# Optimization experiments

Measured on AMD Instinct MI355X. Metric: run time of the kernel, lower is better.

The kernel has to match this reference:

```python
import jax, jax.numpy as jnp
import numpy as np

N_NODES = 100000
N_EDGES = 800000
IN_DIM = 128
HIDDEN_DIM = 256
OUT_DIM = 40


def setup_inputs() -> dict:
    key = jax.random.key(0)
    k_x, k_e, k_w1, k_w2 = jax.random.split(key, 4)
    x = jax.random.normal(k_x, (N_NODES, IN_DIM), dtype=jnp.float32)
    edge_index = jax.random.randint(k_e, (2, N_EDGES), 0, N_NODES, dtype=jnp.int32)
    # Glorot-style init like PyG GCNConv
    s1 = 1.0 / np.sqrt(IN_DIM)
    s2 = 1.0 / np.sqrt(HIDDEN_DIM)
    W1 = jax.random.uniform(k_w1, (IN_DIM, HIDDEN_DIM), dtype=jnp.float32, minval=-s1, maxval=s1)
    b1 = jnp.zeros((HIDDEN_DIM,), dtype=jnp.float32)
    W2 = jax.random.uniform(k_w2, (HIDDEN_DIM, OUT_DIM), dtype=jnp.float32, minval=-s2, maxval=s2)
    b2 = jnp.zeros((OUT_DIM,), dtype=jnp.float32)
    return {"x": x, "edge_index": edge_index, "W1": W1, "b1": b1, "W2": W2, "b2": b2}


def _gcn_conv(x, W, b, src, dst, n_nodes):
    # PyG GCNConv: linear transform, add self-loops, symmetric normalization,
    # scatter-add aggregation, then bias.
    h = x @ W  # [N, F_out]
    loops = jnp.arange(n_nodes, dtype=src.dtype)
    s = jnp.concatenate([src, loops])  # [E+N]
    d = jnp.concatenate([dst, loops])
    deg = jax.ops.segment_sum(jnp.ones_like(d, dtype=h.dtype), d, num_segments=n_nodes)
    dinv = jax.lax.rsqrt(jnp.maximum(deg, 1.0))  # deg >= 1 with self-loops
    norm = dinv[s] * dinv[d]  # [E+N]
    msgs = h[s] * norm[:, None]  # [E+N, F_out] -- dominant memory traffic
    out = jax.ops.segment_sum(msgs, d, num_segments=n_nodes)
    return out + b


def reference(x, edge_index, W1, b1, W2, b2):
    src, dst = edge_index[0], edge_index[1]
    n = x.shape[0]
    h = _gcn_conv(x, W1, b1, src, dst, n)
    h = jax.nn.relu(h)
    # dropout is identity in eval mode
    h = _gcn_conv(h, W2, b2, src, dst, n)
    return jax.nn.log_softmax(h, axis=1)
```

## Files before the change

### kernel.cpp

```cpp
#include <hip/hip_runtime.h>
#include <math.h>

#define N_NODES 100000
#define N_EDGES 800000
#define IN_DIM 128
#define HIDDEN_DIM 256
#define OUT_DIM 40
#define CAP 32
#define SHARD_DIV 12500
#define NPAIRS (N_NODES * 64)
#define T1 (HIDDEN_DIM * IN_DIM)
#define T2 (64 * HIDDEN_DIM)

typedef __attribute__((ext_vector_type(8))) __bf16 bf16x8;
typedef __attribute__((ext_vector_type(4))) float f32x4;

#define FIXSC 131072.0f
#define FIXSC_INV 7.62939453125e-6f

__device__ __forceinline__ unsigned short f2bf(float f) {
    unsigned u = __float_as_uint(f);
    unsigned r = (u + 0x7FFFu + ((u >> 16) & 1u)) >> 16;
    return (unsigned short)r;
}
__device__ __forceinline__ float bflo(unsigned v) { return __uint_as_float(v << 16); }
__device__ __forceinline__ float bfhi(unsigned v) { return __uint_as_float(v & 0xFFFF0000u); }

__device__ __forceinline__ bf16x8 ld_frag16(const unsigned short* p) {
    union { uint4 u; bf16x8 b; } t;
    t.u = *(const uint4*)p;
    return t.b;
}

__global__ __launch_bounds__(256) void fill_kernel(const int* __restrict__ src,
                                                   const int* __restrict__ dst,
                                                   int* __restrict__ cnt,
                                                   int* __restrict__ esrc, int e) {
    int shard = blockIdx.x & 7;
    int i = (blockIdx.x >> 3) * 256 + threadIdx.x;
    if (i < e) {
        int d = dst[i];
        if (d / SHARD_DIV == shard) {
            int p = atomicAdd(&cnt[d], 1);
            if (p < CAP) esrc[d * CAP + p] = src[i];
        }
    }
}

__global__ __launch_bounds__(256) void cast_kernel(const float* __restrict__ x,
                                                   const int* __restrict__ cnt,
                                                   unsigned* __restrict__ xs,
                                                   const float* __restrict__ W1,
                                                   unsigned short* __restrict__ W1t,
                                                   const float* __restrict__ W2,
                                                   unsigned short* __restrict__ W2t) {
    int i = blockIdx.x * 256 + threadIdx.x;
    if (i < NPAIRS) {
        float dn = rsqrtf((float)cnt[i >> 6] + 1.0f) * FIXSC;
        float2 v = ((const float2*)x)[i];
        xs[i] = (unsigned)f2bf(v.x * dn) | ((unsigned)f2bf(v.y * dn) << 16);
    }
    if (i < T1) {
        int n = i >> 7, k = i & 127;
        W1t[i] = f2bf(W1[(size_t)k * HIDDEN_DIM + n]);
    } else if (i < T1 + T2) {
        int j = i - T1;
        int n = j >> 8, k = j & 255;
        float v = (n < OUT_DIM) ? W2[(size_t)k * OUT_DIM + n] : 0.0f;
        W2t[j] = f2bf(v);
    }
}

__global__ __launch_bounds__(256) void aggx_kernel(const unsigned* __restrict__ xs,
                                                   const int* __restrict__ cnt,
                                                   const int* __restrict__ esrc,
                                                   unsigned* __restrict__ aggxb, int n) {
    int wid = (blockIdx.x * 256 + threadIdx.x) >> 6;
    int lane = threadIdx.x & 63;
    if (wid >= n) return;
    int c = cnt[wid];
    int m = c < CAP ? c : CAP;
    unsigned v = xs[(size_t)wid * 64 + lane];
    int ia = (int)bflo(v), ib = (int)bfhi(v);
    int base = wid * CAP;
    int j = 0;
    for (; j + 7 < m; j += 8) {
        int s0 = esrc[base + j],     s1 = esrc[base + j + 1];
        int s2 = esrc[base + j + 2], s3 = esrc[base + j + 3];
        int s4 = esrc[base + j + 4], s5 = esrc[base + j + 5];
        int s6 = esrc[base + j + 6], s7 = esrc[base + j + 7];
        unsigned u0 = xs[(size_t)s0 * 64 + lane];
        unsigned u1 = xs[(size_t)s1 * 64 + lane];
        unsigned u2 = xs[(size_t)s2 * 64 + lane];
        unsigned u3 = xs[(size_t)s3 * 64 + lane];
        unsigned u4 = xs[(size_t)s4 * 64 + lane];
        unsigned u5 = xs[(size_t)s5 * 64 + lane];
        unsigned u6 = xs[(size_t)s6 * 64 + lane];
        unsigned u7 = xs[(size_t)s7 * 64 + lane];
        ia += ((int)bflo(u0) + (int)bflo(u1)) + ((int)bflo(u2) + (int)bflo(u3))
            + ((int)bflo(u4) + (int)bflo(u5)) + ((int)bflo(u6) + (int)bflo(u7));
        ib += ((int)bfhi(u0) + (int)bfhi(u1)) + ((int)bfhi(u2) + (int)bfhi(u3))
            + ((int)bfhi(u4) + (int)bfhi(u5)) + ((int)bfhi(u6) + (int)bfhi(u7));
    }
    for (; j + 3 < m; j += 4) {
        int s0 = esrc[base + j],     s1 = esrc[base + j + 1];
        int s2 = esrc[base + j + 2], s3 = esrc[base + j + 3];
        unsigned u0 = xs[(size_t)s0 * 64 + lane];
        unsigned u1 = xs[(size_t)s1 * 64 + lane];
        unsigned u2 = xs[(size_t)s2 * 64 + lane];
        unsigned u3 = xs[(size_t)s3 * 64 + lane];
        ia += ((int)bflo(u0) + (int)bflo(u1)) + ((int)bflo(u2) + (int)bflo(u3));
        ib += ((int)bfhi(u0) + (int)bfhi(u1)) + ((int)bfhi(u2) + (int)bfhi(u3));
    }
    for (; j < m; j++) {
        unsigned u = xs[(size_t)esrc[base + j] * 64 + lane];
        ia += (int)bflo(u); ib += (int)bfhi(u);
    }
    float k = rsqrtf((float)c + 1.0f) * FIXSC_INV;
    float ax = (float)ia * k, ay = (float)ib * k;
    aggxb[(size_t)wid * 64 + lane] = (unsigned)f2bf(ax) | ((unsigned)f2bf(ay) << 16);
}

#define BSTR 40
#define HSTR 136
__global__ __launch_bounds__(256) void gemm12_kernel(const unsigned short* __restrict__ A,
                                                     const unsigned short* __restrict__ W1t,
                                                     const unsigned short* __restrict__ W2t,
                                                     const float* __restrict__ b1,
                                                     const int* __restrict__ cnt,
                                                     unsigned short* __restrict__ h2s,
                                                     int M) {
    __shared__ __align__(16) unsigned short Bs[256 * BSTR];
    __shared__ __align__(16) unsigned short Hs[4 * 32 * HSTR];
    int tid = threadIdx.x;
    int wv = tid >> 6, lane = tid & 63;
    int quad = lane >> 4, l16 = lane & 15;
    int m0 = blockIdx.x * 128;

    float bv[16];
#pragma unroll
    for (int ct = 0; ct < 16; ct++) bv[ct] = b1[ct * 16 + l16];

    f32x4 zero4 = {0.f, 0.f, 0.f, 0.f};
    f32x4 acc[2][16];
#pragma unroll
    for (int rt = 0; rt < 2; rt++)
#pragma unroll
        for (int ct = 0; ct < 16; ct++) acc[rt][ct] = zero4;

    for (int k0 = 0; k0 < 128; k0 += 32) {
#pragma unroll
        for (int rep = 0; rep < 4; rep++) {
            int lin = rep * 256 + tid;
            int row = lin >> 2, ch = lin & 3;
            *(uint4*)&Bs[row * BSTR + ch * 8] =
                *(const uint4*)&W1t[(size_t)row * 128 + k0 + ch * 8];
        }
        __syncthreads();
        bf16x8 af[2];
#pragma unroll
        for (int rt = 0; rt < 2; rt++) {
            int gm = m0 + wv * 32 + rt * 16 + l16;
            union { uint4 u; bf16x8 b; } cv;
            cv.u = make_uint4(0u, 0u, 0u, 0u);
            if (gm < M) cv.u = *(const uint4*)&A[(size_t)gm * 128 + k0 + quad * 8];
            af[rt] = cv.b;
        }
#pragma unroll
        for (int ct = 0; ct < 16; ct++) {
            bf16x8 bfr = ld_frag16(&Bs[(ct * 16 + l16) * BSTR + quad * 8]);
#pragma unroll
            for (int rt = 0; rt < 2; rt++)
                acc[rt][ct] = __builtin_amdgcn_mfma_f32_16x16x32_bf16(af[rt], bfr, acc[rt][ct], 0, 0, 0);
        }
        __syncthreads();
    }

    unsigned short* hw = &Hs[wv * 32 * HSTR];
    f32x4 acc2[2][4];
#pragma unroll
    for (int rt = 0; rt < 2; rt++)
#pragma unroll
        for (int c2 = 0; c2 < 4; c2++) acc2[rt][c2] = zero4;

#pragma unroll
    for (int chunk = 0; chunk < 2; chunk++) {
#pragma unroll
        for (int rt = 0; rt < 2; rt++)
#pragma unroll
            for (int c8 = 0; c8 < 8; c8++) {
                int ct = chunk * 8 + c8;
#pragma unroll
                for (int r = 0; r < 4; r++) {
                    int row = rt * 16 + quad * 4 + r;
                    float v = fmaxf(acc[rt][ct][r] + bv[ct], 0.0f);
                    hw[row * HSTR + c8 * 16 + l16] = f2bf(v);
                }
            }
#pragma unroll
        for (int kk = 0; kk < 4; kk++) {
            bf16x8 af2[2];
#pragma unroll
            for (int rt = 0; rt < 2; rt++)
                af2[rt] = ld_frag16(&hw[(rt * 16 + l16) * HSTR + kk * 32 + quad * 8]);
#pragma unroll
            for (int c2 = 0; c2 < 4; c2++) {
                bf16x8 bfr = ld_frag16(&W2t[(size_t)(c2 * 16 + l16) * 256 + chunk * 128 + kk * 32 + quad * 8]);
#pragma unroll
                for (int rt = 0; rt < 2; rt++)
                    acc2[rt][c2] = __builtin_amdgcn_mfma_f32_16x16x32_bf16(af2[rt], bfr, acc2[rt][c2], 0, 0, 0);
            }
        }
    }

#pragma unroll
    for (int rt = 0; rt < 2; rt++)
#pragma unroll
        for (int c2 = 0; c2 < 4; c2++) {
            int col = c2 * 16 + l16;
#pragma unroll
            for (int r = 0; r < 4; r++) {
                int gm = m0 + wv * 32 + rt * 16 + quad * 4 + r;
                if (gm < M) {
                    float v = acc2[rt][c2][r] * (rsqrtf((float)cnt[gm] + 1.0f) * FIXSC);
                    h2s[(size_t)gm * 64 + col] = f2bf(v);
                }
            }
        }
}

__global__ __launch_bounds__(256) void agg2_kernel(const unsigned* __restrict__ h2u,
                                                   const int* __restrict__ cnt,
                                                   const int* __restrict__ esrc,
                                                   const float* __restrict__ b2,
                                                   float* __restrict__ out, int n) {
    int wave = (blockIdx.x * 256 + threadIdx.x) >> 6;
    int lane = threadIdx.x & 63;
    int half = lane >> 5, l32 = lane & 31;
    int node = wave * 2 + half;
    if (node >= n) return;
    int c = cnt[node];
    int m = c < CAP ? c : CAP;
    int base = node * CAP;
    unsigned v = h2u[(size_t)node * 32 + l32];
    int ia = (int)bflo(v), ib = (int)bfhi(v);
    int j = 0;
    for (; j + 7 < m; j += 8) {
        int s0 = esrc[base + j],     s1 = esrc[base + j + 1];
        int s2 = esrc[base + j + 2], s3 = esrc[base + j + 3];
        int s4 = esrc[base + j + 4], s5 = esrc[base + j + 5];
        int s6 = esrc[base + j + 6], s7 = esrc[base + j + 7];
        unsigned u0 = h2u[(size_t)s0 * 32 + l32];
        unsigned u1 = h2u[(size_t)s1 * 32 + l32];
        unsigned u2 = h2u[(size_t)s2 * 32 + l32];
        unsigned u3 = h2u[(size_t)s3 * 32 + l32];
        unsigned u4 = h2u[(size_t)s4 * 32 + l32];
        unsigned u5 = h2u[(size_t)s5 * 32 + l32];
        unsigned u6 = h2u[(size_t)s6 * 32 + l32];
        unsigned u7 = h2u[(size_t)s7 * 32 + l32];
        ia += ((int)bflo(u0) + (int)bflo(u1)) + ((int)bflo(u2) + (int)bflo(u3))
            + ((int)bflo(u4) + (int)bflo(u5)) + ((int)bflo(u6) + (int)bflo(u7));
        ib += ((int)bfhi(u0) + (int)bfhi(u1)) + ((int)bfhi(u2) + (int)bfhi(u3))
            + ((int)bfhi(u4) + (int)bfhi(u5)) + ((int)bfhi(u6) + (int)bfhi(u7));
    }
    for (; j + 3 < m; j += 4) {
        int s0 = esrc[base + j],     s1 = esrc[base + j + 1];
        int s2 = esrc[base + j + 2], s3 = esrc[base + j + 3];
        unsigned u0 = h2u[(size_t)s0 * 32 + l32];
        unsigned u1 = h2u[(size_t)s1 * 32 + l32];
        unsigned u2 = h2u[(size_t)s2 * 32 + l32];
        unsigned u3 = h2u[(size_t)s3 * 32 + l32];
        ia += ((int)bflo(u0) + (int)bflo(u1)) + ((int)bflo(u2) + (int)bflo(u3));
        ib += ((int)bfhi(u0) + (int)bfhi(u1)) + ((int)bfhi(u2) + (int)bfhi(u3));
    }
    for (; j < m; j++) {
        unsigned u = h2u[(size_t)esrc[base + j] * 32 + l32];
        ia += (int)bflo(u); ib += (int)bfhi(u);
    }
    float k = rsqrtf((float)c + 1.0f) * FIXSC_INV;
    int f0 = 2 * l32;
    bool a0 = (f0 < OUT_DIM), a1 = (f0 + 1 < OUT_DIM);
    float v0 = a0 ? fmaf((float)ia, k, b2[f0]) : -INFINITY;
    float v1 = a1 ? fmaf((float)ib, k, b2[f0 + 1]) : -INFINITY;
    float mx = fmaxf(v0, v1);
#pragma unroll
    for (int o = 16; o > 0; o >>= 1) mx = fmaxf(mx, __shfl_xor(mx, o));
    float e = (a0 ? __expf(v0 - mx) : 0.0f) + (a1 ? __expf(v1 - mx) : 0.0f);
#pragma unroll
    for (int o = 16; o > 0; o >>= 1) e += __shfl_xor(e, o);
    if (a0) {
        float ls = __logf(e);
        *(float2*)&out[(size_t)node * OUT_DIM + f0] = make_float2(v0 - mx - ls, v1 - mx - ls);
    }
}

extern "C" void kernel_launch(void* const* d_in, const int* in_sizes, int n_in,
                              void* d_out, int out_size, void* d_ws, size_t ws_size,
                              hipStream_t stream) {
    const float* x  = (const float*)d_in[0];
    const int* ei   = (const int*)d_in[1];
    const float* W1 = (const float*)d_in[2];
    const float* b1 = (const float*)d_in[3];
    const float* W2 = (const float*)d_in[4];
    const float* b2 = (const float*)d_in[5];
    float* out = (float*)d_out;

    const int* src = ei;
    const int* dst = ei + N_EDGES;

    char* ws = (char*)d_ws;
    size_t off = 0;
    auto carve = [&](size_t bytes) -> char* {
        char* p = ws + off;
        off = (off + bytes + 255) & ~(size_t)255;
        return p;
    };
    int*      cnt   = (int*)     carve((size_t)N_NODES * 4);
    int*      esrc  = (int*)     carve((size_t)N_NODES * CAP * 4);
    unsigned* xs    = (unsigned*)carve((size_t)N_NODES * 64 * 4);
    unsigned short* W1t = (unsigned short*)carve((size_t)T1 * 2);
    unsigned short* W2t = (unsigned short*)carve((size_t)T2 * 2);
    unsigned* aggxb = (unsigned*)carve((size_t)N_NODES * 64 * 4);
    unsigned short* h2s = (unsigned short*)carve((size_t)N_NODES * 64 * 2);

    hipMemsetAsync(cnt, 0, (size_t)N_NODES * 4, stream);
    fill_kernel<<<((N_EDGES + 255) / 256) * 8, 256, 0, stream>>>(src, dst, cnt, esrc, N_EDGES);
    cast_kernel<<<(NPAIRS + 255) / 256, 256, 0, stream>>>(x, cnt, xs, W1, W1t, W2, W2t);
    aggx_kernel<<<(N_NODES * 64 + 255) / 256, 256, 0, stream>>>(xs, cnt, esrc, aggxb, N_NODES);
    gemm12_kernel<<<(N_NODES + 127) / 128, 256, 0, stream>>>(
        (const unsigned short*)aggxb, W1t, W2t, b1, cnt, h2s, N_NODES);
    agg2_kernel<<<((N_NODES + 1) / 2 * 64 + 255) / 256, 256, 0, stream>>>(
        (const unsigned*)h2s, cnt, esrc, b2, out, N_NODES);
}
```

Before: 279.2 us.

## Shrink gemm12 tile to 16 rows per wave, read W1 fragments from global

The fused two-layer GEMM kernel now gives each wave 16 rows instead of 32, halving the accumulator registers, and declares launch bounds of 4 blocks. W1 fragments are read straight from global/L2 instead of being staged through shared memory, which removes the per-k block barriers. The hidden-layer staging buffer is also smaller and processed in four 64-column chunks. The aim is higher occupancy and fewer syncs, at the cost of W1 reuse dropping by half and more global load traffic per MFMA.

Result: slower. 304.1 us (+8.9%).

```diff
diff --git a/kernel.cpp b/kernel.cpp
--- a/kernel.cpp
+++ b/kernel.cpp
@@ -121,112 +121,83 @@
     aggxb[(size_t)wid * 64 + lane] = (unsigned)f2bf(ax) | ((unsigned)f2bf(ay) << 16);
 }
 
-#define BSTR 40
-#define HSTR 136
-__global__ __launch_bounds__(256) void gemm12_kernel(const unsigned short* __restrict__ A,
-                                                     const unsigned short* __restrict__ W1t,
-                                                     const unsigned short* __restrict__ W2t,
-                                                     const float* __restrict__ b1,
-                                                     const int* __restrict__ cnt,
-                                                     unsigned short* __restrict__ h2s,
-                                                     int M) {
-    __shared__ __align__(16) unsigned short Bs[256 * BSTR];
-    __shared__ __align__(16) unsigned short Hs[4 * 32 * HSTR];
+#define HSTR 72
+__global__ __launch_bounds__(256, 4) void gemm12_kernel(const unsigned short* __restrict__ A,
+                                                        const unsigned short* __restrict__ W1t,
+                                                        const unsigned short* __restrict__ W2t,
+                                                        const float* __restrict__ b1,
+                                                        const int* __restrict__ cnt,
+                                                        unsigned short* __restrict__ h2s,
+                                                        int M) {
+    __shared__ __align__(16) unsigned short Hs[4 * 16 * HSTR];
     int tid = threadIdx.x;
     int wv = tid >> 6, lane = tid & 63;
     int quad = lane >> 4, l16 = lane & 15;
-    int m0 = blockIdx.x * 128;
+    int row0 = blockIdx.x * 64 + wv * 16;
 
     float bv[16];
 #pragma unroll
     for (int ct = 0; ct < 16; ct++) bv[ct] = b1[ct * 16 + l16];
 
     f32x4 zero4 = {0.f, 0.f, 0.f, 0.f};
-    f32x4 acc[2][16];
-#pragma unroll
-    for (int rt = 0; rt < 2; rt++)
-#pragma unroll
-        for (int ct = 0; ct < 16; ct++) acc[rt][ct] = zero4;
-
+    f32x4 acc[16];
+#pragma unroll
+    for (int ct = 0; ct < 16; ct++) acc[ct] = zero4;
+
+#pragma unroll
     for (int k0 = 0; k0 < 128; k0 += 32) {
-#pragma unroll
-        for (int rep = 0; rep < 4; rep++) {
-            int lin = rep * 256 + tid;
-            int row = lin >> 2, ch = lin & 3;
-            *(uint4*)&Bs[row * BSTR + ch * 8] =
-                *(const uint4*)&W1t[(size_t)row * 128 + k0 + ch * 8];
-        }
-        __syncthreads();
-        bf16x8 af[2];
-#pragma unroll
-        for (int rt = 0; rt < 2; rt++) {
-            int gm = m0 + wv * 32 + rt * 16 + l16;
-            union { uint4 u; bf16x8 b; } cv;
-            cv.u = make_uint4(0u, 0u, 0u, 0u);
-            if (gm < M) cv.u = *(const uint4*)&A[(size_t)gm * 128 + k0 + quad * 8];
-            af[rt] = cv.b;
-        }
+        int gm = row0 + l16;
+        union { uint4 u; bf16x8 b; } cv;
+        cv.u = make_uint4(0u, 0u, 0u, 0u);
+        if (gm < M) cv.u = *(const uint4*)&A[(size_t)gm * 128 + k0 + quad * 8];
+        bf16x8 af = cv.b;
 #pragma unroll
         for (int ct = 0; ct < 16; ct++) {
-            bf16x8 bfr = ld_frag16(&Bs[(ct * 16 + l16) * BSTR + quad * 8]);
-#pragma unroll
-            for (int rt = 0; rt < 2; rt++)
-                acc[rt][ct] = __builtin_amdgcn_mfma_f32_16x16x32_bf16(af[rt], bfr, acc[rt][ct], 0, 0, 0);
-        }
-        __syncthreads();
-    }
-
-    unsigned short* hw = &Hs[wv * 32 * HSTR];
-    f32x4 acc2[2][4];
-#pragma unroll
-    for (int rt = 0; rt < 2; rt++)
-#pragma unroll
-        for (int c2 = 0; c2 < 4; c2++) acc2[rt][c2] = zero4;
-
-#pragma unroll
-    for (int chunk = 0; chunk < 2; chunk++) {
-#pragma unroll
-        for (int rt = 0; rt < 2; rt++)
-#pragma unroll
-            for (int c8 = 0; c8 < 8; c8++) {
-                int ct = chunk * 8 + c8;
-#pragma unroll
-                for (int r = 0; r < 4; r++) {
-                    int row = rt * 16 + quad * 4 + r;
-                    float v = fmaxf(acc[rt][ct][r] + bv[ct], 0.0f);
-                    hw[row * HSTR + c8 * 16 + l16] = f2bf(v);
-                }
+            bf16x8 bfr = ld_frag16(&W1t[(size_t)(ct * 16 + l16) * 128 + k0 + quad * 8]);
+            acc[ct] = __builtin_amdgcn_mfma_f32_16x16x32_bf16(af, bfr, acc[ct], 0, 0, 0);
+        }
+    }
+
+    unsigned short* hw = &Hs[wv * 16 * HSTR];
+    f32x4 acc2[4];
+#pragma unroll
+    for (int c2 = 0; c2 < 4; c2++) acc2[c2] = zero4;
+
+#pragma unroll
+    for (int chunk = 0; chunk < 4; chunk++) {
+#pragma unroll
+        for (int cc = 0; cc < 4; cc++) {
+            int ct = chunk * 4 + cc;
+#pragma unroll
+            for (int r = 0; r < 4; r++) {
+                int row = quad * 4 + r;
+                float v = fmaxf(acc[ct][r] + bv[ct], 0.0f);
+                hw[row * HSTR + cc * 16 + l16] = f2bf(v);
             }
-#pragma unroll
-        for (int kk = 0; kk < 4; kk++) {
-            bf16x8 af2[2];
-#pragma unroll
-            for (int rt = 0; rt < 2; rt++)
-                af2[rt] = ld_frag16(&hw[(rt * 16 + l16) * HSTR + kk * 32 + quad * 8]);
+        }
+#pragma unroll
+        for (int kk = 0; kk < 2; kk++) {
+            bf16x8 af2 = ld_frag16(&hw[l16 * HSTR + kk * 32 + quad * 8]);
 #pragma unroll
             for (int c2 = 0; c2 < 4; c2++) {
-                bf16x8 bfr = ld_frag16(&W2t[(size_t)(c2 * 16 + l16) * 256 + chunk * 128 + kk * 32 + quad * 8]);
-#pragma unroll
-                for (int rt = 0; rt < 2; rt++)
-                    acc2[rt][c2] = __builtin_amdgcn_mfma_f32_16x16x32_bf16(af2[rt], bfr, acc2[rt][c2], 0, 0, 0);
+                bf16x8 bfr = ld_frag16(&W2t[(size_t)(c2 * 16 + l16) * 256 + chunk * 64 + kk * 32 + quad * 8]);
+                acc2[c2] = __builtin_amdgcn_mfma_f32_16x16x32_bf16(af2, bfr, acc2[c2], 0, 0, 0);
             }
         }
     }
 
 #pragma unroll
-    for (int rt = 0; rt < 2; rt++)
-#pragma unroll
-        for (int c2 = 0; c2 < 4; c2++) {
-            int col = c2 * 16 + l16;
-#pragma unroll
-            for (int r = 0; r < 4; r++) {
-                int gm = m0 + wv * 32 + rt * 16 + quad * 4 + r;
-                if (gm < M) {
-                    float v = acc2[rt][c2][r] * (rsqrtf((float)cnt[gm] + 1.0f) * FIXSC);
-                    h2s[(size_t)gm * 64 + col] = f2bf(v);
-                }
+    for (int c2 = 0; c2 < 4; c2++) {
+        int col = c2 * 16 + l16;
+#pragma unroll
+        for (int r = 0; r < 4; r++) {
+            int gm = row0 + quad * 4 + r;
+            if (gm < M) {
+                float v = acc2[c2][r] * (rsqrtf((float)cnt[gm] + 1.0f) * FIXSC);
+                h2s[(size_t)gm * 64 + col] = f2bf(v);
             }
         }
+    }
 }
 
 __global__ __launch_bounds__(256) void agg2_kernel(const unsigned* __restrict__ h2u,
@@ -327,7 +298,7 @@
     fill_kernel<<<((N_EDGES + 255) / 256) * 8, 256, 0, stream>>>(src, dst, cnt, esrc, N_EDGES);
     cast_kernel<<<(NPAIRS + 255) / 256, 256, 0, stream>>>(x, cnt, xs, W1, W1t, W2, W2t);
     aggx_kernel<<<(N_NODES * 64 + 255) / 256, 256, 0, stream>>>(xs, cnt, esrc, aggxb, N_NODES);
-    gemm12_kernel<<<(N_NODES + 127) / 128, 256, 0, stream>>>(
+    gemm12_kernel<<<(N_NODES + 63) / 64, 256, 0, stream>>>(
         (const unsigned short*)aggxb, W1t, W2t, b1, cnt, h2s, N_NODES);
     agg2_kernel<<<((N_NODES + 1) / 2 * 64 + 255) / 256, 256, 0, stream>>>(
         (const unsigned*)h2s, cnt, esrc, b2, out, N_NODES);
```
